# Kernel optimization log

Measured on AMD Instinct MI355X. Metric: run time of the kernel, lower is better.

Reference implementation:

```python
import math
import jax, jax.numpy as jnp
import numpy as np

B, T, D = 2048, 50, 256
NEG = -100000.0

def setup_inputs() -> dict:
    key = jax.random.key(0)
    ks = jax.random.split(key, 9)
    return {
        "x": jax.random.normal(ks[0], (B, T, D), dtype=jnp.float32),
        "mask": jax.random.randint(ks[1], (B, T, 1), 0, 2, dtype=jnp.int32),
        "time_decay": jax.random.uniform(ks[2], (B, T, 1), dtype=jnp.float32),
        "Wq": jax.random.normal(ks[3], (D, D), dtype=jnp.float32) * (1.0 / math.sqrt(D)),
        "bq": jax.random.normal(ks[4], (D,), dtype=jnp.float32) * 0.01,
        "Wk": jax.random.normal(ks[5], (D, D), dtype=jnp.float32) * (1.0 / math.sqrt(D)),
        "bk": jax.random.normal(ks[6], (D,), dtype=jnp.float32) * 0.01,
        "Wv": jax.random.normal(ks[7], (D, D), dtype=jnp.float32) * (1.0 / math.sqrt(D)),
        "bv": jax.random.normal(ks[8], (D,), dtype=jnp.float32) * 0.01,
    }

def reference(x, mask, time_decay, Wq, bq, Wk, bk, Wv, bv):
    # PositionalEncoding.forward: elementwise multiply by time-decay (broadcast over d_model)
    x = x * time_decay  # [B,T,D]
    q = jnp.einsum('btd,ed->bte', x, Wq) + bq
    k = jnp.einsum('btd,ed->bte', x, Wk) + bk
    v = jnp.einsum('btd,ed->bte', x, Wv) + bv
    # unusual Q/K-side masking (masked_fill before the matmul)
    keep = mask != 0  # [B,T,1]
    q = jnp.where(keep, q, NEG)
    k = jnp.where(keep, k, NEG)
    score = jnp.einsum('btd,bsd->bts', q, k) / math.sqrt(D)  # [B,T,T]
    score = jax.nn.softmax(score, axis=-1)
    # dropout is identity in eval mode
    out = jnp.einsum('bts,bsd->btd', score, v)  # [B,T,D]
    return out[:, -1, :]  # [B,D]
```

## Files before the change

kernel.cpp:

```cpp
#include <hip/hip_runtime.h>


namespace {
constexpr int kB = 2048;
constexpr int kT = 50;
constexpr int kD = 256;
constexpr double kNeg = -100000.0;
constexpr int oM2 = 0;
constexpr int oWvp = 65536;
constexpr int oV0 = 131072;
constexpr int oC = 131328;
constexpr int oW1 = 131584;
constexpr int oW2 = 131840;
constexpr int oDbl = 132096;
}

__global__ __launch_bounds__(256) void precomp(
    const float* __restrict__ Wq, const float* __restrict__ bq,
    const float* __restrict__ Wk, const float* __restrict__ bk,
    const float* __restrict__ Wv, float* __restrict__ ws) {
  const int t = threadIdx.x;
  const int wave = t >> 6;
  const int lane = t & 63;
  const int blk = blockIdx.x;
  __shared__ float coefL[kD];
  __shared__ double red[3][4];

  if (blk < 256) {
    const int a = blk;
    coefL[t] = Wq[(size_t)t * kD + a];
    __syncthreads();
    const float* kcol = Wk + t;
    float pre[8];
#pragma unroll
    for (int k = 0; k < 8; ++k) pre[k] = kcol[(size_t)k * kD];
    float acc = 0.f;
    for (int j0 = 0; j0 < kD; j0 += 8) {
      float cur[8];
#pragma unroll
      for (int k = 0; k < 8; ++k) cur[k] = pre[k];
      const int nx = (j0 + 8 < kD) ? (j0 + 8) : 0;
#pragma unroll
      for (int k = 0; k < 8; ++k) pre[k] = kcol[(size_t)(nx + k) * kD];
#pragma unroll
      for (int k = 0; k < 8; ++k) acc += coefL[j0 + k] * cur[k];
    }
    ws[oM2 + (a >> 2) * 1024 + 4 * t + (a & 3)] = acc;
  } else if (blk < 258) {
    const float* W = (blk == 256) ? Wk : Wq;
    const float* coef = (blk == 256) ? bq : bk;
    coefL[t] = coef[t];
    __syncthreads();
    const float* col = W + t;
    float pre[8];
#pragma unroll
    for (int k = 0; k < 8; ++k) pre[k] = col[(size_t)k * kD];
    double a0 = 0.0, a1 = 0.0;
    for (int j0 = 0; j0 < kD; j0 += 8) {
      float cur[8];
#pragma unroll
      for (int k = 0; k < 8; ++k) cur[k] = pre[k];
      const int nx = (j0 + 8 < kD) ? (j0 + 8) : 0;
#pragma unroll
      for (int k = 0; k < 8; ++k) pre[k] = col[(size_t)(nx + k) * kD];
#pragma unroll
      for (int k = 0; k < 8; ++k) {
        const double w = (double)cur[k];
        a0 += (double)coefL[j0 + k] * w;
        a1 += w;
      }
    }
    if (blk == 256) {
      ws[oV0 + t] = (float)a0;
      ws[oC + t] = (float)a1;
    } else {
      ws[oW1 + t] = (float)a0;
      ws[oW2 + t] = (float)a1;
      double p0 = (double)bk[t];
      double p1 = (double)bq[t] * (double)bk[t];
      double p2 = (double)bq[t];
#pragma unroll
      for (int off = 32; off; off >>= 1) {
        p0 += __shfl_xor(p0, off);
        p1 += __shfl_xor(p1, off);
        p2 += __shfl_xor(p2, off);
      }
      if (lane == 0) {
        red[0][wave] = p0;
        red[1][wave] = p1;
        red[2][wave] = p2;
      }
      __syncthreads();
      if (t == 0) {
        double* dcw = (double*)(ws + oDbl);
        dcw[0] = red[0][0] + red[0][1] + red[0][2] + red[0][3];
        dcw[1] = red[1][0] + red[1][1] + red[1][2] + red[1][3];
        dcw[2] = red[2][0] + red[2][1] + red[2][2] + red[2][3];
      }
    }
  } else {
    const int d4b = (blk - 258) * 4;
    float4 in[4];
#pragma unroll
    for (int k = 0; k < 4; ++k)
      in[k] = *(const float4*)(Wv + (size_t)t * kD + 4 * (d4b + k));
    float4* Wvp = (float4*)(ws + oWvp);
#pragma unroll
    for (int k = 0; k < 4; ++k) Wvp[(size_t)(d4b + k) * kD + t] = in[k];
  }
}

__global__ __launch_bounds__(64) void fused_main(
    const float* __restrict__ x, const int* __restrict__ mask,
    const float* __restrict__ td, const float* __restrict__ bv,
    const float* __restrict__ ws, float* __restrict__ out) {
  const int lane = threadIdx.x;
  const int b0 = blockIdx.x * 2;
  __shared__ __align__(16) float xsL[2][kD];
  __shared__ __align__(16) float uL[2][kD];
  __shared__ __align__(16) float yL[2][kD];

  const double* dc = (const double*)(ws + oDbl);
  const float4* M2v = (const float4*)(ws + oM2);
  const float4* Wvv = (const float4*)(ws + oWvp);

  const float mtd0 = (lane < kT) ? td[(size_t)(b0 + 0) * kT + lane] : 0.f;
  const float mtd1 = (lane < kT) ? td[(size_t)(b0 + 1) * kT + lane] : 0.f;
  const int mmk0 = (lane < kT) ? mask[(size_t)(b0 + 0) * kT + lane] : 0;
  const int mmk1 = (lane < kT) ? mask[(size_t)(b0 + 1) * kT + lane] : 0;
  const float4 c4 = ((const float4*)(ws + oC))[lane];
  const float4 a1 = ((const float4*)(ws + oW1))[lane];
  const float4 a2 = ((const float4*)(ws + oW2))[lane];

  double Qbk[2], Sq[2];
#pragma unroll
  for (int j = 0; j < 2; ++j) {
    const int b = b0 + j;
    const float tdl = __shfl(j ? mtd1 : mtd0, kT - 1);
    const float4 xv =
        ((const float4*)(x + ((size_t)b * kT + kT - 1) * kD))[lane];
    double s1 = (double)xv.x * a1.x + (double)xv.y * a1.y +
                (double)xv.z * a1.z + (double)xv.w * a1.w;
    double s2 = (double)xv.x * a2.x + (double)xv.y * a2.y +
                (double)xv.z * a2.z + (double)xv.w * a2.w;
#pragma unroll
    for (int off = 32; off; off >>= 1) {
      s1 += __shfl_xor(s1, off);
      s2 += __shfl_xor(s2, off);
    }
    Qbk[j] = (double)tdl * s1 + dc[1];
    Sq[j] = (double)tdl * s2 + dc[2];
    float4 xs;
    xs.x = xv.x * tdl; xs.y = xv.y * tdl;
    xs.z = xv.z * tdl; xs.w = xv.w * tdl;
    *(float4*)(&xsL[j][4 * lane]) = xs;
  }

  {
    float4 A[4], B[4];
#pragma unroll
    for (int g = 0; g < 4; ++g) {
      A[g] = M2v[(size_t)0 * kD + 64 * g + lane];
      B[g] = M2v[(size_t)1 * kD + 64 * g + lane];
    }
    float accU[2][4] = {{0.f, 0.f, 0.f, 0.f}, {0.f, 0.f, 0.f, 0.f}};
    for (int k4 = 0; k4 < 64; k4 += 2) {
      float4 c0[4], c1[4];
#pragma unroll
      for (int g = 0; g < 4; ++g) { c0[g] = A[g]; c1[g] = B[g]; }
      const int n0 = (k4 + 2 < 64) ? k4 + 2 : 0;
      const int n1 = (k4 + 3 < 64) ? k4 + 3 : 1;
#pragma unroll
      for (int g = 0; g < 4; ++g) {
        A[g] = M2v[(size_t)n0 * kD + 64 * g + lane];
        B[g] = M2v[(size_t)n1 * kD + 64 * g + lane];
      }
      const float4 x00 = *(const float4*)(&xsL[0][4 * k4]);
      const float4 x01 = *(const float4*)(&xsL[0][4 * (k4 + 1)]);
      const float4 x10 = *(const float4*)(&xsL[1][4 * k4]);
      const float4 x11 = *(const float4*)(&xsL[1][4 * (k4 + 1)]);
#pragma unroll
      for (int g = 0; g < 4; ++g) {
        accU[0][g] += x00.x * c0[g].x + x00.y * c0[g].y + x00.z * c0[g].z +
                      x00.w * c0[g].w + x01.x * c1[g].x + x01.y * c1[g].y +
                      x01.z * c1[g].z + x01.w * c1[g].w;
        accU[1][g] += x10.x * c0[g].x + x10.y * c0[g].y + x10.z * c0[g].z +
                      x10.w * c0[g].w + x11.x * c1[g].x + x11.y * c1[g].y +
                      x11.z * c1[g].z + x11.w * c1[g].w;
      }
    }
#pragma unroll
    for (int g = 0; g < 4; ++g) {
      const float v0g = ws[oV0 + 64 * g + lane];
      uL[0][64 * g + lane] = accU[0][g] + v0g;
      uL[1][64 * g + lane] = accU[1][g] + v0g;
    }
  }

  const double sbkd = dc[0];
  const double Cbb = 256.0 * 1.0e10 * 0.0625;
#pragma unroll 1
  for (int j = 0; j < 2; ++j) {
    const int b = b0 + j;
    const float mtd = j ? mtd1 : mtd0;
    const int mmk = j ? mmk1 : mmk0;
    const int mqg = __shfl(mmk, kT - 1);
    const float4 u4 = *(const float4*)(&uL[j][4 * lane]);
    const float4 v4 = mqg ? u4 : c4;
    const double Cm = kNeg * Sq[j] * 0.0625;
    const double Qb = Qbk[j];

    const float4* xrow = (const float4*)(x + (size_t)b * kT * kD);
    double m = -1.0e300;
    float l = 0.f;
    float4 y = {0.f, 0.f, 0.f, 0.f};

    float4 n0 = xrow[0 * 64 + lane];
    float4 n1 = xrow[1 * 64 + lane];
    float4 n2 = xrow[2 * 64 + lane];
    float4 n3 = xrow[3 * 64 + lane];
    for (int s = 0; s < 52; s += 4) {
      const float4 r0 = n0, r1 = n1, r2 = n2, r3 = n3;
      {
        const int p0 = (s + 4 < kT) ? s + 4 : kT - 1;
        const int p1 = (s + 5 < kT) ? s + 5 : kT - 1;
        const int p2 = (s + 6 < kT) ? s + 6 : kT - 1;
        const int p3 = (s + 7 < kT) ? s + 7 : kT - 1;
        n0 = xrow[p0 * 64 + lane];
        n1 = xrow[p1 * 64 + lane];
        n2 = xrow[p2 * 64 + lane];
        n3 = xrow[p3 * 64 + lane];
      }
      const int s1i = s + 1, s2i = s + 2, s3i = s + 3;
      const int cc0 = s;
      const int cc1 = (s1i < kT) ? s1i : kT - 1;
      const int cc2 = (s2i < kT) ? s2i : kT - 1;
      const int cc3 = (s3i < kT) ? s3i : kT - 1;
      const float tv0 = __shfl(mtd, cc0);
      const float tv1 = __shfl(mtd, cc1);
      const float tv2 = __shfl(mtd, cc2);
      const float tv3 = __shfl(mtd, cc3);
      float4 a0, aa1, a2v, a3;
      a0.x = r0.x * tv0; a0.y = r0.y * tv0; a0.z = r0.z * tv0; a0.w = r0.w * tv0;
      aa1.x = r1.x * tv1; aa1.y = r1.y * tv1; aa1.z = r1.z * tv1; aa1.w = r1.w * tv1;
      a2v.x = r2.x * tv2; a2v.y = r2.y * tv2; a2v.z = r2.z * tv2; a2v.w = r2.w * tv2;
      a3.x = r3.x * tv3; a3.y = r3.y * tv3; a3.z = r3.z * tv3; a3.w = r3.w * tv3;
      float p0 = a0.x * v4.x + a0.y * v4.y + a0.z * v4.z + a0.w * v4.w;
      float p1 = aa1.x * v4.x + aa1.y * v4.y + aa1.z * v4.z + aa1.w * v4.w;
      float p2 = a2v.x * v4.x + a2v.y * v4.y + a2v.z * v4.z + a2v.w * v4.w;
      float p3 = a3.x * v4.x + a3.y * v4.y + a3.z * v4.z + a3.w * v4.w;
#pragma unroll
      for (int off = 32; off; off >>= 1) {
        p0 += __shfl_xor(p0, off);
        p1 += __shfl_xor(p1, off);
        p2 += __shfl_xor(p2, off);
        p3 += __shfl_xor(p3, off);
      }
      const int ms0 = __shfl(mmk, cc0);
      const int ms1 = __shfl(mmk, cc1);
      const int ms2 = __shfl(mmk, cc2);
      const int ms3 = __shfl(mmk, cc3);
      double sc0, sc1, sc2, sc3;
      if (mqg) {
        sc0 = ms0 ? ((double)p0 + Qb) * 0.0625 : Cm;
        sc1 = ms1 ? ((double)p1 + Qb) * 0.0625 : Cm;
        sc2 = ms2 ? ((double)p2 + Qb) * 0.0625 : Cm;
        sc3 = ms3 ? ((double)p3 + Qb) * 0.0625 : Cm;
      } else {
        sc0 = ms0 ? kNeg * ((double)p0 + sbkd) * 0.0625 : Cbb;
        sc1 = ms1 ? kNeg * ((double)p1 + sbkd) * 0.0625 : Cbb;
        sc2 = ms2 ? kNeg * ((double)p2 + sbkd) * 0.0625 : Cbb;
        sc3 = ms3 ? kNeg * ((double)p3 + sbkd) * 0.0625 : Cbb;
      }
      if (s1i >= kT) sc1 = -1.0e300;
      if (s2i >= kT) sc2 = -1.0e300;
      if (s3i >= kT) sc3 = -1.0e300;
      double mnew = m;
      if (sc0 > mnew) mnew = sc0;
      if (sc1 > mnew) mnew = sc1;
      if (sc2 > mnew) mnew = sc2;
      if (sc3 > mnew) mnew = sc3;
      const float al = expf((float)(m - mnew));
      const float e0 = expf((float)(sc0 - mnew));
      const float e1 = expf((float)(sc1 - mnew));
      const float e2 = expf((float)(sc2 - mnew));
      const float e3 = expf((float)(sc3 - mnew));
      m = mnew;
      l = l * al + e0 + e1 + e2 + e3;
      y.x = y.x * al + e0 * a0.x + e1 * aa1.x + e2 * a2v.x + e3 * a3.x;
      y.y = y.y * al + e0 * a0.y + e1 * aa1.y + e2 * a2v.y + e3 * a3.y;
      y.z = y.z * al + e0 * a0.z + e1 * aa1.z + e2 * a2v.z + e3 * a3.z;
      y.w = y.w * al + e0 * a0.w + e1 * aa1.w + e2 * a2v.w + e3 * a3.w;
    }
    const float inv = 1.0f / l;
    y.x *= inv; y.y *= inv; y.z *= inv; y.w *= inv;
    *(float4*)(&yL[j][4 * lane]) = y;
  }

  {
    float4 A[4], B[4];
#pragma unroll
    for (int g = 0; g < 4; ++g) {
      A[g] = Wvv[(size_t)0 * kD + 64 * g + lane];
      B[g] = Wvv[(size_t)1 * kD + 64 * g + lane];
    }
    float accO[2][4] = {{0.f, 0.f, 0.f, 0.f}, {0.f, 0.f, 0.f, 0.f}};
    for (int k4 = 0; k4 < 64; k4 += 2) {
      float4 c0[4], c1[4];
#pragma unroll
      for (int g = 0; g < 4; ++g) { c0[g] = A[g]; c1[g] = B[g]; }
      const int n0 = (k4 + 2 < 64) ? k4 + 2 : 0;
      const int n1 = (k4 + 3 < 64) ? k4 + 3 : 1;
#pragma unroll
      for (int g = 0; g < 4; ++g) {
        A[g] = Wvv[(size_t)n0 * kD + 64 * g + lane];
        B[g] = Wvv[(size_t)n1 * kD + 64 * g + lane];
      }
      const float4 y00 = *(const float4*)(&yL[0][4 * k4]);
      const float4 y01 = *(const float4*)(&yL[0][4 * (k4 + 1)]);
      const float4 y10 = *(const float4*)(&yL[1][4 * k4]);
      const float4 y11 = *(const float4*)(&yL[1][4 * (k4 + 1)]);
#pragma unroll
      for (int g = 0; g < 4; ++g) {
        accO[0][g] += y00.x * c0[g].x + y00.y * c0[g].y + y00.z * c0[g].z +
                      y00.w * c0[g].w + y01.x * c1[g].x + y01.y * c1[g].y +
                      y01.z * c1[g].z + y01.w * c1[g].w;
        accO[1][g] += y10.x * c0[g].x + y10.y * c0[g].y + y10.z * c0[g].z +
                      y10.w * c0[g].w + y11.x * c1[g].x + y11.y * c1[g].y +
                      y11.z * c1[g].z + y11.w * c1[g].w;
      }
    }
#pragma unroll
    for (int g = 0; g < 4; ++g) {
      const float bvg = bv[64 * g + lane];
      out[(size_t)(b0 + 0) * kD + 64 * g + lane] = accO[0][g] + bvg;
      out[(size_t)(b0 + 1) * kD + 64 * g + lane] = accO[1][g] + bvg;
    }
  }
}

extern "C" void kernel_launch(void* const* d_in, const int* in_sizes, int n_in,
                              void* d_out, int out_size, void* d_ws,
                              size_t ws_size, hipStream_t stream) {
  const float* x = (const float*)d_in[0];
  const int* mask = (const int*)d_in[1];
  const float* td = (const float*)d_in[2];
  const float* Wq = (const float*)d_in[3];
  const float* bq = (const float*)d_in[4];
  const float* Wk = (const float*)d_in[5];
  const float* bk = (const float*)d_in[6];
  const float* Wv = (const float*)d_in[7];
  const float* bv = (const float*)d_in[8];
  float* ws = (float*)d_ws;
  float* out = (float*)d_out;
  (void)in_sizes; (void)n_in; (void)out_size; (void)ws_size;

  hipLaunchKernelGGL(precomp, dim3(274), dim3(256), 0, stream, Wq, bq, Wk, bk,
                     Wv, ws);
  hipLaunchKernelGGL(fused_main, dim3(kB / 2), dim3(64), 0, stream, x, mask,
                     td, bv, (const float*)ws, out);
}
```

Measured before the change: 209.2 us.

## Spread fused_main across four waves with split-sequence softmax merge

The main kernel goes from one wave per block to four waves per block. The two 256x256 matvec stages now split their output columns across the waves. The attention scan is split into two halves of the sequence per batch item, with partial max, sum and accumulator values merged through shared memory in online-softmax style. This targets the serialized per-wave work and low parallelism of the old 64-thread block, at the cost of extra __syncthreads barriers and shared-memory traffic.

```diff
diff --git a/kernel.cpp b/kernel.cpp
--- a/kernel.cpp
+++ b/kernel.cpp
@@ -110,33 +110,38 @@
   }
 }
 
-__global__ __launch_bounds__(64) void fused_main(
+__global__ __launch_bounds__(256) void fused_main(
     const float* __restrict__ x, const int* __restrict__ mask,
     const float* __restrict__ td, const float* __restrict__ bv,
     const float* __restrict__ ws, float* __restrict__ out) {
-  const int lane = threadIdx.x;
+  const int tid = threadIdx.x;
+  const int lane = tid & 63;
+  const int w = tid >> 6;
   const int b0 = blockIdx.x * 2;
   __shared__ __align__(16) float xsL[2][kD];
   __shared__ __align__(16) float uL[2][kD];
   __shared__ __align__(16) float yL[2][kD];
+  __shared__ __align__(16) float ypart[2][2][kD];
+  __shared__ double mpart[2][2];
+  __shared__ float lpart[2][2];
+  __shared__ double dScal[2][2];
 
   const double* dc = (const double*)(ws + oDbl);
   const float4* M2v = (const float4*)(ws + oM2);
   const float4* Wvv = (const float4*)(ws + oWvp);
 
-  const float mtd0 = (lane < kT) ? td[(size_t)(b0 + 0) * kT + lane] : 0.f;
-  const float mtd1 = (lane < kT) ? td[(size_t)(b0 + 1) * kT + lane] : 0.f;
-  const int mmk0 = (lane < kT) ? mask[(size_t)(b0 + 0) * kT + lane] : 0;
-  const int mmk1 = (lane < kT) ? mask[(size_t)(b0 + 1) * kT + lane] : 0;
+  const int ja = w >> 1;
+  const int h = w & 1;
+  const float mtdA = (lane < kT) ? td[(size_t)(b0 + ja) * kT + lane] : 0.f;
+  const int mmkA = (lane < kT) ? mask[(size_t)(b0 + ja) * kT + lane] : 0;
   const float4 c4 = ((const float4*)(ws + oC))[lane];
-  const float4 a1 = ((const float4*)(ws + oW1))[lane];
-  const float4 a2 = ((const float4*)(ws + oW2))[lane];
-
-  double Qbk[2], Sq[2];
-#pragma unroll
-  for (int j = 0; j < 2; ++j) {
+
+  if (h == 0) {
+    const int j = ja;
     const int b = b0 + j;
-    const float tdl = __shfl(j ? mtd1 : mtd0, kT - 1);
+    const float tdl = __shfl(mtdA, kT - 1);
+    const float4 a1 = ((const float4*)(ws + oW1))[lane];
+    const float4 a2 = ((const float4*)(ws + oW2))[lane];
     const float4 xv =
         ((const float4*)(x + ((size_t)b * kT + kT - 1) * kD))[lane];
     double s1 = (double)xv.x * a1.x + (double)xv.y * a1.y +
@@ -148,88 +153,78 @@
       s1 += __shfl_xor(s1, off);
       s2 += __shfl_xor(s2, off);
     }
-    Qbk[j] = (double)tdl * s1 + dc[1];
-    Sq[j] = (double)tdl * s2 + dc[2];
+    if (lane == 0) {
+      dScal[j][0] = (double)tdl * s1 + dc[1];
+      dScal[j][1] = (double)tdl * s2 + dc[2];
+    }
     float4 xs;
     xs.x = xv.x * tdl; xs.y = xv.y * tdl;
     xs.z = xv.z * tdl; xs.w = xv.w * tdl;
     *(float4*)(&xsL[j][4 * lane]) = xs;
   }
+  __syncthreads();
 
   {
-    float4 A[4], B[4];
-#pragma unroll
-    for (int g = 0; g < 4; ++g) {
-      A[g] = M2v[(size_t)0 * kD + 64 * g + lane];
-      B[g] = M2v[(size_t)1 * kD + 64 * g + lane];
-    }
-    float accU[2][4] = {{0.f, 0.f, 0.f, 0.f}, {0.f, 0.f, 0.f, 0.f}};
+    const int col = 64 * w + lane;
+    float4 A = M2v[col];
+    float4 B = M2v[256 + col];
+    float acc0 = 0.f, acc1 = 0.f;
     for (int k4 = 0; k4 < 64; k4 += 2) {
-      float4 c0[4], c1[4];
-#pragma unroll
-      for (int g = 0; g < 4; ++g) { c0[g] = A[g]; c1[g] = B[g]; }
+      const float4 c0 = A, c1 = B;
       const int n0 = (k4 + 2 < 64) ? k4 + 2 : 0;
       const int n1 = (k4 + 3 < 64) ? k4 + 3 : 1;
-#pragma unroll
-      for (int g = 0; g < 4; ++g) {
-        A[g] = M2v[(size_t)n0 * kD + 64 * g + lane];
-        B[g] = M2v[(size_t)n1 * kD + 64 * g + lane];
-      }
+      A = M2v[(size_t)n0 * 256 + col];
+      B = M2v[(size_t)n1 * 256 + col];
       const float4 x00 = *(const float4*)(&xsL[0][4 * k4]);
       const float4 x01 = *(const float4*)(&xsL[0][4 * (k4 + 1)]);
       const float4 x10 = *(const float4*)(&xsL[1][4 * k4]);
       const float4 x11 = *(const float4*)(&xsL[1][4 * (k4 + 1)]);
-#pragma unroll
-      for (int g = 0; g < 4; ++g) {
-        accU[0][g] += x00.x * c0[g].x + x00.y * c0[g].y + x00.z * c0[g].z +
-                      x00.w * c0[g].w + x01.x * c1[g].x + x01.y * c1[g].y +
-                      x01.z * c1[g].z + x01.w * c1[g].w;
-        accU[1][g] += x10.x * c0[g].x + x10.y * c0[g].y + x10.z * c0[g].z +
-                      x10.w * c0[g].w + x11.x * c1[g].x + x11.y * c1[g].y +
-                      x11.z * c1[g].z + x11.w * c1[g].w;
-      }
-    }
-#pragma unroll
-    for (int g = 0; g < 4; ++g) {
-      const float v0g = ws[oV0 + 64 * g + lane];
-      uL[0][64 * g + lane] = accU[0][g] + v0g;
-      uL[1][64 * g + lane] = accU[1][g] + v0g;
-    }
-  }
-
-  const double sbkd = dc[0];
-  const double Cbb = 256.0 * 1.0e10 * 0.0625;
-#pragma unroll 1
-  for (int j = 0; j < 2; ++j) {
+      acc0 += x00.x * c0.x + x00.y * c0.y + x00.z * c0.z + x00.w * c0.w +
+              x01.x * c1.x + x01.y * c1.y + x01.z * c1.z + x01.w * c1.w;
+      acc1 += x10.x * c0.x + x10.y * c0.y + x10.z * c0.z + x10.w * c0.w +
+              x11.x * c1.x + x11.y * c1.y + x11.z * c1.z + x11.w * c1.w;
+    }
+    const float v0g = ws[oV0 + col];
+    uL[0][col] = acc0 + v0g;
+    uL[1][col] = acc1 + v0g;
+  }
+  __syncthreads();
+
+  {
+    const int j = ja;
     const int b = b0 + j;
-    const float mtd = j ? mtd1 : mtd0;
-    const int mmk = j ? mmk1 : mmk0;
+    const float mtd = mtdA;
+    const int mmk = mmkA;
     const int mqg = __shfl(mmk, kT - 1);
     const float4 u4 = *(const float4*)(&uL[j][4 * lane]);
     const float4 v4 = mqg ? u4 : c4;
-    const double Cm = kNeg * Sq[j] * 0.0625;
-    const double Qb = Qbk[j];
+    const double Qb = dScal[j][0];
+    const double Cm = kNeg * dScal[j][1] * 0.0625;
+    const double sbkd = dc[0];
+    const double Cbb = 256.0 * 1.0e10 * 0.0625;
+    const int sbeg = h ? 24 : 0;
+    const int slim = h ? 52 : 24;
 
     const float4* xrow = (const float4*)(x + (size_t)b * kT * kD);
     double m = -1.0e300;
     float l = 0.f;
     float4 y = {0.f, 0.f, 0.f, 0.f};
 
-    float4 n0 = xrow[0 * 64 + lane];
-    float4 n1 = xrow[1 * 64 + lane];
-    float4 n2 = xrow[2 * 64 + lane];
-    float4 n3 = xrow[3 * 64 + lane];
-    for (int s = 0; s < 52; s += 4) {
+    float4 n0 = xrow[(size_t)(sbeg + 0) * 64 + lane];
+    float4 n1 = xrow[(size_t)(sbeg + 1) * 64 + lane];
+    float4 n2 = xrow[(size_t)(sbeg + 2) * 64 + lane];
+    float4 n3 = xrow[(size_t)(sbeg + 3) * 64 + lane];
+    for (int s = sbeg; s < slim; s += 4) {
       const float4 r0 = n0, r1 = n1, r2 = n2, r3 = n3;
       {
         const int p0 = (s + 4 < kT) ? s + 4 : kT - 1;
         const int p1 = (s + 5 < kT) ? s + 5 : kT - 1;
         const int p2 = (s + 6 < kT) ? s + 6 : kT - 1;
         const int p3 = (s + 7 < kT) ? s + 7 : kT - 1;
-        n0 = xrow[p0 * 64 + lane];
-        n1 = xrow[p1 * 64 + lane];
-        n2 = xrow[p2 * 64 + lane];
-        n3 = xrow[p3 * 64 + lane];
+        n0 = xrow[(size_t)p0 * 64 + lane];
+        n1 = xrow[(size_t)p1 * 64 + lane];
+        n2 = xrow[(size_t)p2 * 64 + lane];
+        n3 = xrow[(size_t)p3 * 64 + lane];
       }
       const int s1i = s + 1, s2i = s + 2, s3i = s + 3;
       const int cc0 = s;
@@ -292,50 +287,56 @@
       y.z = y.z * al + e0 * a0.z + e1 * aa1.z + e2 * a2v.z + e3 * a3.z;
       y.w = y.w * al + e0 * a0.w + e1 * aa1.w + e2 * a2v.w + e3 * a3.w;
     }
+    if (lane == 0) {
+      mpart[j][h] = m;
+      lpart[j][h] = l;
+    }
+    *(float4*)(&ypart[j][h][4 * lane]) = y;
+  }
+  __syncthreads();
+
+  if (h == 0) {
+    const int j = ja;
+    const double m0 = mpart[j][0], m1 = mpart[j][1];
+    const double M = (m0 > m1) ? m0 : m1;
+    const float e0 = expf((float)(m0 - M));
+    const float e1 = expf((float)(m1 - M));
+    const float l = lpart[j][0] * e0 + lpart[j][1] * e1;
     const float inv = 1.0f / l;
-    y.x *= inv; y.y *= inv; y.z *= inv; y.w *= inv;
-    *(float4*)(&yL[j][4 * lane]) = y;
-  }
+    const float4 y0 = *(const float4*)(&ypart[j][0][4 * lane]);
+    const float4 y1 = *(const float4*)(&ypart[j][1][4 * lane]);
+    float4 yv;
+    yv.x = (y0.x * e0 + y1.x * e1) * inv;
+    yv.y = (y0.y * e0 + y1.y * e1) * inv;
+    yv.z = (y0.z * e0 + y1.z * e1) * inv;
+    yv.w = (y0.w * e0 + y1.w * e1) * inv;
+    *(float4*)(&yL[j][4 * lane]) = yv;
+  }
+  __syncthreads();
 
   {
-    float4 A[4], B[4];
-#pragma unroll
-    for (int g = 0; g < 4; ++g) {
-      A[g] = Wvv[(size_t)0 * kD + 64 * g + lane];
-      B[g] = Wvv[(size_t)1 * kD + 64 * g + lane];
-    }
-    float accO[2][4] = {{0.f, 0.f, 0.f, 0.f}, {0.f, 0.f, 0.f, 0.f}};
+    const int col = 64 * w + lane;
+    float4 A = Wvv[col];
+    float4 B = Wvv[256 + col];
+    float acc0 = 0.f, acc1 = 0.f;
     for (int k4 = 0; k4 < 64; k4 += 2) {
-      float4 c0[4], c1[4];
-#pragma unroll
-      for (int g = 0; g < 4; ++g) { c0[g] = A[g]; c1[g] = B[g]; }
+      const float4 c0 = A, c1 = B;
       const int n0 = (k4 + 2 < 64) ? k4 + 2 : 0;
       const int n1 = (k4 + 3 < 64) ? k4 + 3 : 1;
-#pragma unroll
-      for (int g = 0; g < 4; ++g) {
-        A[g] = Wvv[(size_t)n0 * kD + 64 * g + lane];
-        B[g] = Wvv[(size_t)n1 * kD + 64 * g + lane];
-      }
+      A = Wvv[(size_t)n0 * 256 + col];
+      B = Wvv[(size_t)n1 * 256 + col];
       const float4 y00 = *(const float4*)(&yL[0][4 * k4]);
       const float4 y01 = *(const float4*)(&yL[0][4 * (k4 + 1)]);
       const float4 y10 = *(const float4*)(&yL[1][4 * k4]);
       const float4 y11 = *(const float4*)(&yL[1][4 * (k4 + 1)]);
-#pragma unroll
-      for (int g = 0; g < 4; ++g) {
-        accO[0][g] += y00.x * c0[g].x + y00.y * c0[g].y + y00.z * c0[g].z +
-                      y00.w * c0[g].w + y01.x * c1[g].x + y01.y * c1[g].y +
-                      y01.z * c1[g].z + y01.w * c1[g].w;
-        accO[1][g] += y10.x * c0[g].x + y10.y * c0[g].y + y10.z * c0[g].z +
-                      y10.w * c0[g].w + y11.x * c1[g].x + y11.y * c1[g].y +
-                      y11.z * c1[g].z + y11.w * c1[g].w;
-      }
-    }
-#pragma unroll
-    for (int g = 0; g < 4; ++g) {
-      const float bvg = bv[64 * g + lane];
-      out[(size_t)(b0 + 0) * kD + 64 * g + lane] = accO[0][g] + bvg;
-      out[(size_t)(b0 + 1) * kD + 64 * g + lane] = accO[1][g] + bvg;
-    }
+      acc0 += y00.x * c0.x + y00.y * c0.y + y00.z * c0.z + y00.w * c0.w +
+              y01.x * c1.x + y01.y * c1.y + y01.z * c1.z + y01.w * c1.w;
+      acc1 += y10.x * c0.x + y10.y * c0.y + y10.z * c0.z + y10.w * c0.w +
+              y11.x * c1.x + y11.y * c1.y + y11.z * c1.z + y11.w * c1.w;
+    }
+    const float bvg = bv[col];
+    out[(size_t)(b0 + 0) * kD + col] = acc0 + bvg;
+    out[(size_t)(b0 + 1) * kD + col] = acc1 + bvg;
   }
 }
 
@@ -357,6 +358,6 @@
 
   hipLaunchKernelGGL(precomp, dim3(274), dim3(256), 0, stream, Wq, bq, Wk, bk,
                      Wv, ws);
-  hipLaunchKernelGGL(fused_main, dim3(kB / 2), dim3(64), 0, stream, x, mask,
+  hipLaunchKernelGGL(fused_main, dim3(kB / 2), dim3(256), 0, stream, x, mask,
                      td, bv, (const float*)ws, out);
 }
```

After: 197.6 us. 1.06x faster.
